# Performance work log

Measured on AMD Instinct MI355X. Metric: run time of the kernel, lower is better.

## Reference

```python
import jax, jax.numpy as jnp
import numpy as np

N_MICS = 192
OVERLAP = 1024
WINDOW = 524288
SPEED_OF_SOUND = 343000.0  # mm/s
FS = 768000.0


def setup_inputs() -> dict:
    key = jax.random.key(0)
    k1, k2, k3 = jax.random.split(key, 3)
    pos = jax.random.normal(k1, (1, 3), dtype=jnp.float32) * 100.0 + jnp.array([[363.0, -344.0, 1607.0]], dtype=jnp.float32)
    mic_pos = jax.random.uniform(k2, (N_MICS, 3), dtype=jnp.float32) * 100.0  # mm, spread ~100mm -> delays << OVERLAP
    buffer = jax.random.normal(k3, (N_MICS, OVERLAP + WINDOW), dtype=jnp.float32)
    return {"pos": pos, "mic_pos": mic_pos, "buffer": buffer}


def reference(pos, mic_pos, buffer):
    # distances: cdist((1,3),(M,3)) -> (M,)
    diff = pos[:, None, :] - mic_pos[None, :, :]
    distances = jnp.sqrt(jnp.sum(diff * diff, axis=-1))[0]  # (M,)
    distances = distances - distances.max()  # <= 0
    delay = -distances / SPEED_OF_SOUND * FS / 16.0  # >= 0, in samples
    delay_int = delay.astype(jnp.int32)  # trunc == floor for nonneg (matches torch .long())
    delay_frac = delay - delay_int.astype(delay.dtype)  # (M,)
    # gather indices: (M, W)
    idx = jnp.arange(WINDOW, dtype=jnp.int32)[None, :] + OVERLAP - delay_int[:, None]
    v1 = jnp.take_along_axis(buffer, idx, axis=1)       # (M, W)
    v2 = jnp.take_along_axis(buffer, idx - 1, axis=1)   # (M, W)
    f = delay_frac[:, None]
    delayed = v1 * (1.0 - f) + v2 * f
    return delayed.mean(axis=0)  # (W,)
```

## Files before the change

kernel.cpp:

```cpp
#include <hip/hip_runtime.h>

#define N_MICS  192
#define OVERLAP 1024
#define WINDOW  524288
#define ROWLEN  (OVERLAP + WINDOW)
#define SPT     4
#define BLK     256

__global__ __launch_bounds__(BLK) void tdbf_kernel(
    const float* __restrict__ pos,
    const float* __restrict__ mic_pos,
    const float* __restrict__ buf,
    float* __restrict__ out)
{
    __shared__ float s_dist[N_MICS];
    __shared__ int   s_off[N_MICS];
    __shared__ float s_df[N_MICS];

    const int tid = threadIdx.x;

    if (tid < N_MICS) {
        float dx = __fsub_rn(pos[0], mic_pos[tid * 3 + 0]);
        float dy = __fsub_rn(pos[1], mic_pos[tid * 3 + 1]);
        float dz = __fsub_rn(pos[2], mic_pos[tid * 3 + 2]);
        float ss = __fadd_rn(__fadd_rn(__fmul_rn(dx, dx), __fmul_rn(dy, dy)),
                             __fmul_rn(dz, dz));
        s_dist[tid] = __fsqrt_rn(ss);
    }
    __syncthreads();
    if (tid < N_MICS) {
        float mx = s_dist[0];
        for (int i = 1; i < N_MICS; ++i) mx = fmaxf(mx, s_dist[i]);
        float dd = __fsub_rn(s_dist[tid], mx);
        float delay = __fmul_rn(
                          __fmul_rn(__fdiv_rn(-dd, 343000.0f), 768000.0f),
                          0.0625f);
        int di = (int)delay;
        s_off[tid] = tid * ROWLEN + OVERLAP - di;
        s_df[tid]  = __fsub_rn(delay, (float)di);
    }
    __syncthreads();

    const int t4 = (blockIdx.x * BLK + tid) * SPT;
    float a0 = 0.0f, a1 = 0.0f, a2 = 0.0f, a3 = 0.0f;

    #pragma unroll 6
    for (int m = 0; m < N_MICS; ++m) {
        const int   off = __builtin_amdgcn_readfirstlane(s_off[m]);
        const float f   = __uint_as_float(
                              __builtin_amdgcn_readfirstlane(__float_as_uint(s_df[m])));
        const float* p  = buf + off + t4;
        const float vm1 = p[-1];
        const float v0  = p[0];
        const float v1  = p[1];
        const float v2  = p[2];
        const float v3  = p[3];
        const float g   = 1.0f - f;
        a0 = fmaf(v0, g, fmaf(vm1, f, a0));
        a1 = fmaf(v1, g, fmaf(v0,  f, a1));
        a2 = fmaf(v2, g, fmaf(v1,  f, a2));
        a3 = fmaf(v3, g, fmaf(v2,  f, a3));
    }

    const float inv = 1.0f / (float)N_MICS;
    float4 o;
    o.x = a0 * inv; o.y = a1 * inv; o.z = a2 * inv; o.w = a3 * inv;
    *reinterpret_cast<float4*>(out + t4) = o;
}

extern "C" void kernel_launch(void* const* d_in, const int* in_sizes, int n_in,
                              void* d_out, int out_size, void* d_ws, size_t ws_size,
                              hipStream_t stream) {
    const float* pos     = (const float*)d_in[0];
    const float* mic_pos = (const float*)d_in[1];
    const float* buf     = (const float*)d_in[2];
    float* out           = (float*)d_out;

    dim3 grid(WINDOW / (BLK * SPT));
    dim3 block(BLK);
    tdbf_kernel<<<grid, block, 0, stream>>>(pos, mic_pos, buf, out);
}
```

Before: 77.55 us.

## Group mics by alignment residue to use aligned float4 loads

Sorts microphones into four groups by the residue of their start offset mod 4, then for each group issues two 16-byte aligned float4 loads and picks the needed five elements at compile time. This replaces five scalar unaligned loads per mic with two vector loads, cutting load instruction count. It adds a block-level counting sort in the prologue with extra syncs, and the grouped loops have runtime bounds that may hinder unrolling. Summation order across mics changes, so floating-point rounding differs slightly.

```diff
diff --git a/kernel.cpp b/kernel.cpp
--- a/kernel.cpp
+++ b/kernel.cpp
@@ -14,8 +14,13 @@
     float* __restrict__ out)
 {
     __shared__ float s_dist[N_MICS];
+    __shared__ int   s_r[N_MICS];
+    __shared__ int   s_offA[N_MICS];
+    __shared__ float s_dfA[N_MICS];
     __shared__ int   s_off[N_MICS];
     __shared__ float s_df[N_MICS];
+    __shared__ int   s_cnt[4];
+    __shared__ int   s_start[5];
 
     const int tid = threadIdx.x;
 
@@ -36,30 +41,59 @@
                           __fmul_rn(__fdiv_rn(-dd, 343000.0f), 768000.0f),
                           0.0625f);
         int di = (int)delay;
-        s_off[tid] = tid * ROWLEN + OVERLAP - di;
-        s_df[tid]  = __fsub_rn(delay, (float)di);
+        int off = tid * ROWLEN + OVERLAP - di;
+        s_offA[tid] = off;
+        s_dfA[tid]  = __fsub_rn(delay, (float)di);
+        s_r[tid]    = (off - 1) & 3;
+    }
+    __syncthreads();
+    if (tid < 4) {
+        int c = 0;
+        for (int j = 0; j < N_MICS; ++j) c += (s_r[j] == tid);
+        s_cnt[tid] = c;
+    }
+    __syncthreads();
+    if (tid == 0) {
+        s_start[0] = 0;
+        for (int g = 0; g < 4; ++g) s_start[g + 1] = s_start[g] + s_cnt[g];
+    }
+    __syncthreads();
+    if (tid < N_MICS) {
+        const int myr = s_r[tid];
+        int rank = 0;
+        for (int j = 0; j < N_MICS; ++j) rank += (j < tid) & (s_r[j] == myr);
+        const int p = s_start[myr] + rank;
+        s_off[p] = s_offA[tid];
+        s_df[p]  = s_dfA[tid];
     }
     __syncthreads();
 
     const int t4 = (blockIdx.x * BLK + tid) * SPT;
     float a0 = 0.0f, a1 = 0.0f, a2 = 0.0f, a3 = 0.0f;
 
-    #pragma unroll 6
-    for (int m = 0; m < N_MICS; ++m) {
-        const int   off = __builtin_amdgcn_readfirstlane(s_off[m]);
-        const float f   = __uint_as_float(
-                              __builtin_amdgcn_readfirstlane(__float_as_uint(s_df[m])));
-        const float* p  = buf + off + t4;
-        const float vm1 = p[-1];
-        const float v0  = p[0];
-        const float v1  = p[1];
-        const float v2  = p[2];
-        const float v3  = p[3];
-        const float g   = 1.0f - f;
-        a0 = fmaf(v0, g, fmaf(vm1, f, a0));
-        a1 = fmaf(v1, g, fmaf(v0,  f, a1));
-        a2 = fmaf(v2, g, fmaf(v1,  f, a2));
-        a3 = fmaf(v3, g, fmaf(v2,  f, a3));
+    #pragma unroll
+    for (int g = 0; g < 4; ++g) {
+        const int iBeg = __builtin_amdgcn_readfirstlane(s_start[g]);
+        const int iEnd = __builtin_amdgcn_readfirstlane(s_start[g + 1]);
+        #pragma unroll 4
+        for (int i = iBeg; i < iEnd; ++i) {
+            const int   off = __builtin_amdgcn_readfirstlane(s_off[i]);
+            const float f   = __uint_as_float(
+                                  __builtin_amdgcn_readfirstlane(__float_as_uint(s_df[i])));
+            const int A = off + t4 - 1 - g;
+            const float4 wa = *reinterpret_cast<const float4*>(buf + A);
+            const float4 wb = *reinterpret_cast<const float4*>(buf + A + 4);
+            float vm1, v0, v1, v2, v3;
+            if      (g == 0) { vm1 = wa.x; v0 = wa.y; v1 = wa.z; v2 = wa.w; v3 = wb.x; }
+            else if (g == 1) { vm1 = wa.y; v0 = wa.z; v1 = wa.w; v2 = wb.x; v3 = wb.y; }
+            else if (g == 2) { vm1 = wa.z; v0 = wa.w; v1 = wb.x; v2 = wb.y; v3 = wb.z; }
+            else             { vm1 = wa.w; v0 = wb.x; v1 = wb.y; v2 = wb.z; v3 = wb.w; }
+            const float gg = 1.0f - f;
+            a0 = fmaf(v0, gg, fmaf(vm1, f, a0));
+            a1 = fmaf(v1, gg, fmaf(v0,  f, a1));
+            a2 = fmaf(v2, gg, fmaf(v1,  f, a2));
+            a3 = fmaf(v3, gg, fmaf(v2,  f, a3));
+        }
     }
 
     const float inv = 1.0f / (float)N_MICS;
```

Result: slower. 132.2 us (+70.5%).

## Split mic reduction across two blocks with workspace and separate reduce kernel

Applied to the files above, without the earlier changes.

Each block now computes 8 outputs per thread over half of the microphones, writes partial sums to a workspace, and a second kernel adds the two halves and scales by the mic count. This keeps the block count the same while doubling samples per thread, so each mic iteration has more independent loads in flight and the p[-1] overlap is amortised over more outputs. It costs an extra kernel launch plus a workspace write and read of two window-sized arrays. A single-kernel path remains as a fallback when the workspace is too small.

```diff
diff --git a/kernel.cpp b/kernel.cpp
--- a/kernel.cpp
+++ b/kernel.cpp
@@ -4,21 +4,12 @@
 #define OVERLAP 1024
 #define WINDOW  524288
 #define ROWLEN  (OVERLAP + WINDOW)
-#define SPT     4
 #define BLK     256
 
-__global__ __launch_bounds__(BLK) void tdbf_kernel(
-    const float* __restrict__ pos,
-    const float* __restrict__ mic_pos,
-    const float* __restrict__ buf,
-    float* __restrict__ out)
+__device__ __forceinline__ void compute_delays(
+    const float* __restrict__ pos, const float* __restrict__ mic_pos,
+    float* s_dist, int* s_off, float* s_df, int tid)
 {
-    __shared__ float s_dist[N_MICS];
-    __shared__ int   s_off[N_MICS];
-    __shared__ float s_df[N_MICS];
-
-    const int tid = threadIdx.x;
-
     if (tid < N_MICS) {
         float dx = __fsub_rn(pos[0], mic_pos[tid * 3 + 0]);
         float dy = __fsub_rn(pos[1], mic_pos[tid * 3 + 1]);
@@ -40,31 +31,101 @@
         s_df[tid]  = __fsub_rn(delay, (float)di);
     }
     __syncthreads();
+}
 
-    const int t4 = (blockIdx.x * BLK + tid) * SPT;
-    float a0 = 0.0f, a1 = 0.0f, a2 = 0.0f, a3 = 0.0f;
+#define RFL_I(x) __builtin_amdgcn_readfirstlane(x)
+#define RFL_F(x) __uint_as_float(__builtin_amdgcn_readfirstlane(__float_as_uint(x)))
 
+__global__ __launch_bounds__(BLK) void tdbf_partial(
+    const float* __restrict__ pos,
+    const float* __restrict__ mic_pos,
+    const float* __restrict__ buf,
+    float* __restrict__ ws)
+{
+    __shared__ float s_dist[N_MICS];
+    __shared__ int   s_off[N_MICS];
+    __shared__ float s_df[N_MICS];
+    const int tid = threadIdx.x;
+    compute_delays(pos, mic_pos, s_dist, s_off, s_df, tid);
+
+    const int half = blockIdx.x & 1;
+    const int tblk = blockIdx.x >> 1;
+    const int t8   = (tblk * BLK + tid) * 8;
+    const int mBeg = half * (N_MICS / 2);
+
+    float a0 = 0.f, a1 = 0.f, a2 = 0.f, a3 = 0.f;
+    float a4 = 0.f, a5 = 0.f, a6 = 0.f, a7 = 0.f;
+
+    #pragma unroll 4
+    for (int mi = 0; mi < N_MICS / 2; ++mi) {
+        const int   off = RFL_I(s_off[mBeg + mi]);
+        const float f   = RFL_F(s_df[mBeg + mi]);
+        const float* p  = buf + off + t8;
+        const float vm1 = p[-1];
+        const float v0 = p[0], v1 = p[1], v2 = p[2], v3 = p[3];
+        const float v4 = p[4], v5 = p[5], v6 = p[6], v7 = p[7];
+        const float g  = 1.0f - f;
+        a0 = fmaf(v0, g, fmaf(vm1, f, a0));
+        a1 = fmaf(v1, g, fmaf(v0,  f, a1));
+        a2 = fmaf(v2, g, fmaf(v1,  f, a2));
+        a3 = fmaf(v3, g, fmaf(v2,  f, a3));
+        a4 = fmaf(v4, g, fmaf(v3,  f, a4));
+        a5 = fmaf(v5, g, fmaf(v4,  f, a5));
+        a6 = fmaf(v6, g, fmaf(v5,  f, a6));
+        a7 = fmaf(v7, g, fmaf(v6,  f, a7));
+    }
+
+    float* w = ws + (size_t)half * WINDOW + t8;
+    float4 o0; o0.x = a0; o0.y = a1; o0.z = a2; o0.w = a3;
+    float4 o1; o1.x = a4; o1.y = a5; o1.z = a6; o1.w = a7;
+    *reinterpret_cast<float4*>(w)     = o0;
+    *reinterpret_cast<float4*>(w + 4) = o1;
+}
+
+__global__ __launch_bounds__(BLK) void tdbf_reduce(
+    const float* __restrict__ ws, float* __restrict__ out)
+{
+    const int i = (blockIdx.x * BLK + threadIdx.x) * 4;
+    const float4 x = *reinterpret_cast<const float4*>(ws + i);
+    const float4 y = *reinterpret_cast<const float4*>(ws + WINDOW + i);
+    const float inv = 1.0f / (float)N_MICS;
+    float4 o;
+    o.x = (x.x + y.x) * inv;
+    o.y = (x.y + y.y) * inv;
+    o.z = (x.z + y.z) * inv;
+    o.w = (x.w + y.w) * inv;
+    *reinterpret_cast<float4*>(out + i) = o;
+}
+
+__global__ __launch_bounds__(BLK) void tdbf_mono(
+    const float* __restrict__ pos,
+    const float* __restrict__ mic_pos,
+    const float* __restrict__ buf,
+    float* __restrict__ out)
+{
+    __shared__ float s_dist[N_MICS];
+    __shared__ int   s_off[N_MICS];
+    __shared__ float s_df[N_MICS];
+    const int tid = threadIdx.x;
+    compute_delays(pos, mic_pos, s_dist, s_off, s_df, tid);
+
+    const int t4 = (blockIdx.x * BLK + tid) * 4;
+    float a0 = 0.f, a1 = 0.f, a2 = 0.f, a3 = 0.f;
     #pragma unroll 6
     for (int m = 0; m < N_MICS; ++m) {
-        const int   off = __builtin_amdgcn_readfirstlane(s_off[m]);
-        const float f   = __uint_as_float(
-                              __builtin_amdgcn_readfirstlane(__float_as_uint(s_df[m])));
+        const int   off = RFL_I(s_off[m]);
+        const float f   = RFL_F(s_df[m]);
         const float* p  = buf + off + t4;
         const float vm1 = p[-1];
-        const float v0  = p[0];
-        const float v1  = p[1];
-        const float v2  = p[2];
-        const float v3  = p[3];
-        const float g   = 1.0f - f;
+        const float v0 = p[0], v1 = p[1], v2 = p[2], v3 = p[3];
+        const float g  = 1.0f - f;
         a0 = fmaf(v0, g, fmaf(vm1, f, a0));
         a1 = fmaf(v1, g, fmaf(v0,  f, a1));
         a2 = fmaf(v2, g, fmaf(v1,  f, a2));
         a3 = fmaf(v3, g, fmaf(v2,  f, a3));
     }
-
     const float inv = 1.0f / (float)N_MICS;
-    float4 o;
-    o.x = a0 * inv; o.y = a1 * inv; o.z = a2 * inv; o.w = a3 * inv;
+    float4 o; o.x = a0 * inv; o.y = a1 * inv; o.z = a2 * inv; o.w = a3 * inv;
     *reinterpret_cast<float4*>(out + t4) = o;
 }
 
@@ -76,7 +137,15 @@
     const float* buf     = (const float*)d_in[2];
     float* out           = (float*)d_out;
 
-    dim3 grid(WINDOW / (BLK * SPT));
-    dim3 block(BLK);
-    tdbf_kernel<<<grid, block, 0, stream>>>(pos, mic_pos, buf, out);
+    const size_t ws_needed = (size_t)2 * WINDOW * sizeof(float);
+    if (ws_size >= ws_needed) {
+        float* ws = (float*)d_ws;
+        dim3 grid(2 * WINDOW / (BLK * 8));
+        tdbf_partial<<<grid, dim3(BLK), 0, stream>>>(pos, mic_pos, buf, ws);
+        dim3 rgrid(WINDOW / (BLK * 4));
+        tdbf_reduce<<<rgrid, dim3(BLK), 0, stream>>>(ws, out);
+    } else {
+        dim3 grid(WINDOW / (BLK * 4));
+        tdbf_mono<<<grid, dim3(BLK), 0, stream>>>(pos, mic_pos, buf, out);
+    }
 }
```

New measurement: 82.20 us. 6.0% more time.
